# Kernel optimization log

Measured on AMD Instinct MI355X. Metric: run time of the kernel, lower is better.

## Reference

```python
import jax, jax.numpy as jnp
import numpy as np

ROPE_BASE = 10000.0
NEG_INF = -1e30


def _rope(x, pos):
    # x: [B, Hx, D], pos: [B] int32. Rotate-half RoPE (non-interleaved).
    D = x.shape[-1]
    inv_freq = 1.0 / (ROPE_BASE ** (jnp.arange(0, D, 2, dtype=jnp.float32) / D))  # [D/2]
    ang = pos.astype(jnp.float32)[:, None] * inv_freq[None, :]                    # [B, D/2]
    emb = jnp.concatenate([ang, ang], axis=-1)                                    # [B, D]
    cos = jnp.cos(emb)[:, None, :]
    sin = jnp.sin(emb)[:, None, :]
    x1, x2 = x[..., : D // 2], x[..., D // 2 :]
    rotated = jnp.concatenate([-x2, x1], axis=-1)
    return x * cos + rotated * sin


def setup_inputs() -> dict:
    key = jax.random.key(0)
    ks = jax.random.split(key, 7)
    B, H, KVH, D = 32, 32, 8, 128
    BLOCK_SIZE, MAX_BLOCKS = 16, 128
    NUM_BLOCKS = B * MAX_BLOCKS  # 4096, disjoint blocks per sequence
    MAX_CTX = BLOCK_SIZE * MAX_BLOCKS  # 2048
    query = jax.random.normal(ks[0], (B, H, D), dtype=jnp.float32)
    new_k = jax.random.normal(ks[1], (B, KVH, D), dtype=jnp.float32)
    new_v = jax.random.normal(ks[2], (B, KVH, D), dtype=jnp.float32)
    k_cache = jax.random.normal(ks[3], (NUM_BLOCKS, BLOCK_SIZE, KVH, D), dtype=jnp.float32)
    v_cache = jax.random.normal(ks[4], (NUM_BLOCKS, BLOCK_SIZE, KVH, D), dtype=jnp.float32)
    block_table = jnp.arange(B * MAX_BLOCKS, dtype=jnp.int32).reshape(B, MAX_BLOCKS)
    context_lens = jnp.clip(jax.random.randint(ks[5], (B,), 0, MAX_CTX, dtype=jnp.int32), 1, MAX_CTX)
    return {"query": query, "key": new_k, "value": new_v,
            "k_cache": k_cache, "v_cache": v_cache,
            "block_table": block_table, "context_lens": context_lens}


def reference(query, key, value, k_cache, v_cache, block_table, context_lens):
    B, H, D = query.shape
    KVH = key.shape[1]
    G = H // KVH  # GQA group size
    block_size = k_cache.shape[1]
    max_blocks = block_table.shape[1]
    S = max_blocks * block_size
    scale = D ** -0.5

    # RoPE at position = context_lens (as in the original module)
    q_rot = _rope(query, context_lens)  # [B, H, D]
    k_rot = _rope(key, context_lens)    # [B, KVH, D]

    # Store new KV at token index context_lens - 1 via block table (paged scatter)
    tok = context_lens - 1
    blk = jnp.take_along_axis(block_table, (tok // block_size)[:, None], axis=1)[:, 0]  # [B]
    off = tok % block_size
    k_cache = k_cache.at[blk, off].set(k_rot)
    v_cache = v_cache.at[blk, off].set(value)

    # Gather per-sequence pages: [B, max_blocks, block_size, KVH, D] -> [B, S, KVH, D]
    K = k_cache[block_table].reshape(B, S, KVH, D)
    V = v_cache[block_table].reshape(B, S, KVH, D)

    # Single-query attention over valid context (positions < context_lens)
    qg = q_rot.reshape(B, KVH, G, D)
    scores = jnp.einsum("bkgd,bskd->bkgs", qg, K) * scale  # [B, KVH, G, S]
    valid = jnp.arange(S, dtype=jnp.int32)[None, :] < context_lens[:, None]  # [B, S]
    scores = jnp.where(valid[:, None, None, :], scores, NEG_INF)
    probs = jax.nn.softmax(scores, axis=-1)
    out = jnp.einsum("bkgs,bskd->bkgd", probs, V).reshape(B, H, D)
    return out
```

## Files before the change

kernel.cpp:

```cpp
#include <hip/hip_runtime.h>
#include <math.h>

#define BATCH 32
#define NH 32
#define NKVH 8
#define GRP 4
#define HD 128
#define BLKSZ 16
#define MAXB 128
#define PART 128
#define NPART 16
#define SCALE 0.08838834764831845f
#define NEGINF (-1e30f)

#define WS_QROT 0
#define WS_ML   (BATCH*NH*HD)
#define WS_OP   (WS_ML + BATCH*NKVH*GRP*NPART*2)

__global__ __launch_bounds__(128)
void prep(const float* __restrict__ q,
          const float* __restrict__ nk,
          const float* __restrict__ nv,
          float* __restrict__ kc,
          float* __restrict__ vc,
          const int* __restrict__ btab,
          const int* __restrict__ ctx,
          float* __restrict__ ws) {
    int b = blockIdx.x;
    int t = threadIdx.x;
    int L = ctx[b];
    __shared__ float cs[64], sn[64];
    if (t < 64) {
        double f = pow(10000.0, -(double)t / 64.0);
        double a = (double)L * f;
        cs[t] = (float)cos(a);
        sn[t] = (float)sin(a);
    }
    __syncthreads();
    float c = cs[t & 63], s = sn[t & 63];
    for (int h = 0; h < NH; ++h) {
        const float* qp = q + ((size_t)b * NH + h) * HD;
        float x = qp[t], y = qp[t ^ 64];
        float r = (t < 64) ? (x * c - y * s) : (x * c + y * s);
        ws[WS_QROT + ((size_t)b * NH + h) * HD + t] = r * SCALE;
    }
    int tok = L - 1;
    int blk = btab[b * MAXB + (tok >> 4)];
    int off = tok & 15;
    for (int kh = 0; kh < NKVH; ++kh) {
        const float* kp = nk + ((size_t)b * NKVH + kh) * HD;
        float x = kp[t], y = kp[t ^ 64];
        float r = (t < 64) ? (x * c - y * s) : (x * c + y * s);
        size_t row = (((size_t)blk * BLKSZ + off) * NKVH + kh) * HD;
        kc[row + t] = r;
        vc[row + t] = nv[((size_t)b * NKVH + kh) * HD + t];
    }
}

__global__ __launch_bounds__(256)
void attn(const float* __restrict__ kc,
          const float* __restrict__ vc,
          const int* __restrict__ ctx,
          const int* __restrict__ btab,
          float* __restrict__ ws)
{
    int part = blockIdx.x, kvh = blockIdx.y, b = blockIdx.z;
    int L = ctx[b];
    int start = part * PART;
    if (start >= L) return;
    int end = min(start + PART, L);
    int n = end - start;

    int tid = threadIdx.x;
    int hw = tid >> 5;
    int hl = tid & 31;
    int wave = tid >> 6, lane = tid & 63;

    __shared__ int   bts[PART / BLKSZ];
    __shared__ float qs[GRP][HD];
    __shared__ float sc[GRP][PART];
    __shared__ float oacc[4][GRP][HD];

    if (tid < PART / BLKSZ)
        bts[tid] = btab[b * MAXB + (start >> 4) + tid];
    {
        const float* qrot = ws + WS_QROT + ((size_t)b * NH + kvh * GRP) * HD;
        ((float2*)&qs[0][0])[tid] = ((const float2*)qrot)[tid];
    }
    __syncthreads();

    float4 qa[GRP];
#pragma unroll
    for (int g = 0; g < GRP; ++g)
        qa[g] = *(const float4*)(&qs[g][4 * hl]);

    const size_t koff = (size_t)kvh * HD + 4 * hl;

    int i = start + hw;
    for (; i + 24 < end; i += 32) {
        int s0 = i, s1 = i + 8, s2 = i + 16, s3 = i + 24;
        float4 k0 = *(const float4*)(kc + ((size_t)bts[(s0 - start) >> 4] << 14) + ((s0 & 15) << 10) + koff);
        float4 k1 = *(const float4*)(kc + ((size_t)bts[(s1 - start) >> 4] << 14) + ((s1 & 15) << 10) + koff);
        float4 k2 = *(const float4*)(kc + ((size_t)bts[(s2 - start) >> 4] << 14) + ((s2 & 15) << 10) + koff);
        float4 k3 = *(const float4*)(kc + ((size_t)bts[(s3 - start) >> 4] << 14) + ((s3 & 15) << 10) + koff);
        float p0[GRP], p1[GRP], p2[GRP], p3[GRP];
#pragma unroll
        for (int g = 0; g < GRP; ++g) {
            p0[g] = qa[g].x * k0.x + qa[g].y * k0.y + qa[g].z * k0.z + qa[g].w * k0.w;
            p1[g] = qa[g].x * k1.x + qa[g].y * k1.y + qa[g].z * k1.z + qa[g].w * k1.w;
            p2[g] = qa[g].x * k2.x + qa[g].y * k2.y + qa[g].z * k2.z + qa[g].w * k2.w;
            p3[g] = qa[g].x * k3.x + qa[g].y * k3.y + qa[g].z * k3.z + qa[g].w * k3.w;
        }
#pragma unroll
        for (int off = 16; off >= 1; off >>= 1) {
#pragma unroll
            for (int g = 0; g < GRP; ++g) {
                p0[g] += __shfl_xor(p0[g], off, 32);
                p1[g] += __shfl_xor(p1[g], off, 32);
                p2[g] += __shfl_xor(p2[g], off, 32);
                p3[g] += __shfl_xor(p3[g], off, 32);
            }
        }
        if (hl == 0) {
#pragma unroll
            for (int g = 0; g < GRP; ++g) {
                sc[g][s0 - start] = p0[g];
                sc[g][s1 - start] = p1[g];
                sc[g][s2 - start] = p2[g];
                sc[g][s3 - start] = p3[g];
            }
        }
    }
    for (; i < end; i += 8) {
        float4 k0 = *(const float4*)(kc + ((size_t)bts[(i - start) >> 4] << 14) + ((i & 15) << 10) + koff);
        float p0[GRP];
#pragma unroll
        for (int g = 0; g < GRP; ++g)
            p0[g] = qa[g].x * k0.x + qa[g].y * k0.y + qa[g].z * k0.z + qa[g].w * k0.w;
#pragma unroll
        for (int off = 16; off >= 1; off >>= 1)
#pragma unroll
            for (int g = 0; g < GRP; ++g)
                p0[g] += __shfl_xor(p0[g], off, 32);
        if (hl == 0)
#pragma unroll
            for (int g = 0; g < GRP; ++g)
                sc[g][i - start] = p0[g];
    }
    __syncthreads();

    {
        int g = wave;
        float m = NEGINF;
        for (int j = lane; j < n; j += 64) m = fmaxf(m, sc[g][j]);
#pragma unroll
        for (int off = 32; off >= 1; off >>= 1) m = fmaxf(m, __shfl_xor(m, off));
        float sum = 0.f;
        for (int j = lane; j < n; j += 64) {
            float e = __expf(sc[g][j] - m);
            sc[g][j] = e;
            sum += e;
        }
#pragma unroll
        for (int off = 32; off >= 1; off >>= 1) sum += __shfl_xor(sum, off);
        if (lane == 0) {
            size_t mlidx = ((((size_t)b * NKVH + kvh) * GRP + g) * NPART + part) * 2;
            ws[WS_ML + mlidx]     = m;
            ws[WS_ML + mlidx + 1] = sum;
        }
    }
    __syncthreads();

    float2 acc[GRP];
#pragma unroll
    for (int g = 0; g < GRP; ++g) acc[g] = make_float2(0.f, 0.f);

    const size_t voff = (size_t)kvh * HD + 2 * lane;
    int t0 = start + (wave << 6);
    int tend = min(t0 + 64, end);
    int t = t0;
    for (; t + 3 < tend; t += 4) {
        float2 v0 = *(const float2*)(vc + ((size_t)bts[(t     - start) >> 4] << 14) + (( t      & 15) << 10) + voff);
        float2 v1 = *(const float2*)(vc + ((size_t)bts[(t + 1 - start) >> 4] << 14) + (((t + 1) & 15) << 10) + voff);
        float2 v2 = *(const float2*)(vc + ((size_t)bts[(t + 2 - start) >> 4] << 14) + (((t + 2) & 15) << 10) + voff);
        float2 v3 = *(const float2*)(vc + ((size_t)bts[(t + 3 - start) >> 4] << 14) + (((t + 3) & 15) << 10) + voff);
#pragma unroll
        for (int g = 0; g < GRP; ++g) {
            float4 e = *(const float4*)(&sc[g][t - start]);
            acc[g].x += e.x * v0.x; acc[g].y += e.x * v0.y;
            acc[g].x += e.y * v1.x; acc[g].y += e.y * v1.y;
            acc[g].x += e.z * v2.x; acc[g].y += e.z * v2.y;
            acc[g].x += e.w * v3.x; acc[g].y += e.w * v3.y;
        }
    }
    for (; t < tend; ++t) {
        float2 v0 = *(const float2*)(vc + ((size_t)bts[(t - start) >> 4] << 14) + ((t & 15) << 10) + voff);
#pragma unroll
        for (int g = 0; g < GRP; ++g) {
            float e = sc[g][t - start];
            acc[g].x += e * v0.x; acc[g].y += e * v0.y;
        }
    }
#pragma unroll
    for (int g = 0; g < GRP; ++g)
        *(float2*)&oacc[wave][g][2 * lane] = acc[g];
    __syncthreads();

    for (int o = tid; o < GRP * HD; o += 256) {
        int g = o >> 7, d = o & 127;
        float ssum = oacc[0][g][d] + oacc[1][g][d] + oacc[2][g][d] + oacc[3][g][d];
        ws[WS_OP + ((((size_t)b * NKVH + kvh) * GRP + g) * NPART + part) * HD + d] = ssum;
    }
}

__global__ __launch_bounds__(128)
void attn_reduce(const int* __restrict__ ctx,
                 const float* __restrict__ ws,
                 float* __restrict__ out) {
    int bh = blockIdx.x;
    int b = bh >> 5;
    int h = bh & 31;
    int kvh = h >> 2, g = h & 3;
    int L = ctx[b];
    int np = min(NPART, (L + PART - 1) / PART);
    size_t base = (((size_t)b * NKVH + kvh) * GRP + g) * NPART;
    float M = NEGINF;
    for (int p = 0; p < np; ++p)
        M = fmaxf(M, ws[WS_ML + (base + p) * 2]);
    float w_[NPART];
    float Lsum = 0.f;
    for (int p = 0; p < np; ++p) {
        float e = __expf(ws[WS_ML + (base + p) * 2] - M);
        w_[p] = e;
        Lsum += e * ws[WS_ML + (base + p) * 2 + 1];
    }
    float inv = 1.0f / Lsum;
    int d = threadIdx.x;
    float acc = 0.f;
    for (int p = 0; p < np; ++p)
        acc += w_[p] * ws[WS_OP + (base + p) * HD + d];
    out[((size_t)b * NH + h) * HD + d] = acc * inv;
}

extern "C" void kernel_launch(void* const* d_in, const int* in_sizes, int n_in,
                              void* d_out, int out_size, void* d_ws, size_t ws_size,
                              hipStream_t stream) {
    const float* q    = (const float*)d_in[0];
    const float* nk   = (const float*)d_in[1];
    const float* nv   = (const float*)d_in[2];
    float*       kc   = (float*)d_in[3];
    float*       vc   = (float*)d_in[4];
    const int*   btab = (const int*)d_in[5];
    const int*   ctx  = (const int*)d_in[6];
    float* out = (float*)d_out;
    float* ws  = (float*)d_ws;

    prep<<<dim3(BATCH), dim3(128), 0, stream>>>(q, nk, nv, kc, vc, btab, ctx, ws);
    attn<<<dim3(NPART, NKVH, BATCH), dim3(256), 0, stream>>>(kc, vc, ctx, btab, ws);
    attn_reduce<<<dim3(BATCH * NH), dim3(128), 0, stream>>>(ctx, ws, out);
}
```

Baseline: 490.5 us.

## Stop writing new KV into cache; inject new token in attention and use nontemporal loads

The prep kernel no longer scatters the rotated key and new value into the paged caches. It stores the rotated key in workspace, and the attention kernel handles the last token specially by reading the new key and value directly. Cache loads switch to nontemporal builtins to reduce cache pollution. This drops the in-place cache mutation, so repeated calls no longer depend on modified inputs, and it adds a small branch in the last partition.

```diff
diff --git a/kernel.cpp b/kernel.cpp
--- a/kernel.cpp
+++ b/kernel.cpp
@@ -14,16 +14,23 @@
 #define NEGINF (-1e30f)
 
 #define WS_QROT 0
-#define WS_ML   (BATCH*NH*HD)
+#define WS_KROT (BATCH*NH*HD)
+#define WS_ML   (WS_KROT + BATCH*NKVH*HD)
 #define WS_OP   (WS_ML + BATCH*NKVH*GRP*NPART*2)
+
+typedef float f32x4 __attribute__((ext_vector_type(4)));
+typedef float f32x2 __attribute__((ext_vector_type(2)));
+
+__device__ __forceinline__ f32x4 ldnt4(const float* p) {
+    return __builtin_nontemporal_load((const f32x4*)p);
+}
+__device__ __forceinline__ f32x2 ldnt2(const float* p) {
+    return __builtin_nontemporal_load((const f32x2*)p);
+}
 
 __global__ __launch_bounds__(128)
 void prep(const float* __restrict__ q,
           const float* __restrict__ nk,
-          const float* __restrict__ nv,
-          float* __restrict__ kc,
-          float* __restrict__ vc,
-          const int* __restrict__ btab,
           const int* __restrict__ ctx,
           float* __restrict__ ws) {
     int b = blockIdx.x;
@@ -44,22 +51,18 @@
         float r = (t < 64) ? (x * c - y * s) : (x * c + y * s);
         ws[WS_QROT + ((size_t)b * NH + h) * HD + t] = r * SCALE;
     }
-    int tok = L - 1;
-    int blk = btab[b * MAXB + (tok >> 4)];
-    int off = tok & 15;
     for (int kh = 0; kh < NKVH; ++kh) {
         const float* kp = nk + ((size_t)b * NKVH + kh) * HD;
         float x = kp[t], y = kp[t ^ 64];
         float r = (t < 64) ? (x * c - y * s) : (x * c + y * s);
-        size_t row = (((size_t)blk * BLKSZ + off) * NKVH + kh) * HD;
-        kc[row + t] = r;
-        vc[row + t] = nv[((size_t)b * NKVH + kh) * HD + t];
+        ws[WS_KROT + ((size_t)b * NKVH + kh) * HD + t] = r;
     }
 }
 
 __global__ __launch_bounds__(256)
 void attn(const float* __restrict__ kc,
           const float* __restrict__ vc,
+          const float* __restrict__ nv,
           const int* __restrict__ ctx,
           const int* __restrict__ btab,
           float* __restrict__ ws)
@@ -70,6 +73,8 @@
     if (start >= L) return;
     int end = min(start + PART, L);
     int n = end - start;
+    bool hasNew = (end == L);
+    int endC = end - (hasNew ? 1 : 0);
 
     int tid = threadIdx.x;
     int hw = tid >> 5;
@@ -97,12 +102,12 @@
     const size_t koff = (size_t)kvh * HD + 4 * hl;
 
     int i = start + hw;
-    for (; i + 24 < end; i += 32) {
+    for (; i + 24 < endC; i += 32) {
         int s0 = i, s1 = i + 8, s2 = i + 16, s3 = i + 24;
-        float4 k0 = *(const float4*)(kc + ((size_t)bts[(s0 - start) >> 4] << 14) + ((s0 & 15) << 10) + koff);
-        float4 k1 = *(const float4*)(kc + ((size_t)bts[(s1 - start) >> 4] << 14) + ((s1 & 15) << 10) + koff);
-        float4 k2 = *(const float4*)(kc + ((size_t)bts[(s2 - start) >> 4] << 14) + ((s2 & 15) << 10) + koff);
-        float4 k3 = *(const float4*)(kc + ((size_t)bts[(s3 - start) >> 4] << 14) + ((s3 & 15) << 10) + koff);
+        f32x4 k0 = ldnt4(kc + ((size_t)bts[(s0 - start) >> 4] << 14) + ((s0 & 15) << 10) + koff);
+        f32x4 k1 = ldnt4(kc + ((size_t)bts[(s1 - start) >> 4] << 14) + ((s1 & 15) << 10) + koff);
+        f32x4 k2 = ldnt4(kc + ((size_t)bts[(s2 - start) >> 4] << 14) + ((s2 & 15) << 10) + koff);
+        f32x4 k3 = ldnt4(kc + ((size_t)bts[(s3 - start) >> 4] << 14) + ((s3 & 15) << 10) + koff);
         float p0[GRP], p1[GRP], p2[GRP], p3[GRP];
 #pragma unroll
         for (int g = 0; g < GRP; ++g) {
@@ -131,8 +136,8 @@
             }
         }
     }
-    for (; i < end; i += 8) {
-        float4 k0 = *(const float4*)(kc + ((size_t)bts[(i - start) >> 4] << 14) + ((i & 15) << 10) + koff);
+    for (; i < endC; i += 8) {
+        f32x4 k0 = ldnt4(kc + ((size_t)bts[(i - start) >> 4] << 14) + ((i & 15) << 10) + koff);
         float p0[GRP];
 #pragma unroll
         for (int g = 0; g < GRP; ++g)
@@ -146,6 +151,17 @@
 #pragma unroll
             for (int g = 0; g < GRP; ++g)
                 sc[g][i - start] = p0[g];
+    }
+
+    if (hasNew) {
+        int g = wave;
+        const float* kn = ws + WS_KROT + ((size_t)b * NKVH + kvh) * HD;
+        float2 kv = *(const float2*)(kn + 2 * lane);
+        float2 qv = *(const float2*)(&qs[g][2 * lane]);
+        float p = qv.x * kv.x + qv.y * kv.y;
+#pragma unroll
+        for (int off = 32; off >= 1; off >>= 1) p += __shfl_xor(p, off);
+        if (lane == 0) sc[g][n - 1] = p;
     }
     __syncthreads();
 
@@ -177,13 +193,13 @@
 
     const size_t voff = (size_t)kvh * HD + 2 * lane;
     int t0 = start + (wave << 6);
-    int tend = min(t0 + 64, end);
+    int tend = min(t0 + 64, endC);
     int t = t0;
     for (; t + 3 < tend; t += 4) {
-        float2 v0 = *(const float2*)(vc + ((size_t)bts[(t     - start) >> 4] << 14) + (( t      & 15) << 10) + voff);
-        float2 v1 = *(const float2*)(vc + ((size_t)bts[(t + 1 - start) >> 4] << 14) + (((t + 1) & 15) << 10) + voff);
-        float2 v2 = *(const float2*)(vc + ((size_t)bts[(t + 2 - start) >> 4] << 14) + (((t + 2) & 15) << 10) + voff);
-        float2 v3 = *(const float2*)(vc + ((size_t)bts[(t + 3 - start) >> 4] << 14) + (((t + 3) & 15) << 10) + voff);
+        f32x2 v0 = ldnt2(vc + ((size_t)bts[(t     - start) >> 4] << 14) + (( t      & 15) << 10) + voff);
+        f32x2 v1 = ldnt2(vc + ((size_t)bts[(t + 1 - start) >> 4] << 14) + (((t + 1) & 15) << 10) + voff);
+        f32x2 v2 = ldnt2(vc + ((size_t)bts[(t + 2 - start) >> 4] << 14) + (((t + 2) & 15) << 10) + voff);
+        f32x2 v3 = ldnt2(vc + ((size_t)bts[(t + 3 - start) >> 4] << 14) + (((t + 3) & 15) << 10) + voff);
 #pragma unroll
         for (int g = 0; g < GRP; ++g) {
             float4 e = *(const float4*)(&sc[g][t - start]);
@@ -194,11 +210,19 @@
         }
     }
     for (; t < tend; ++t) {
-        float2 v0 = *(const float2*)(vc + ((size_t)bts[(t - start) >> 4] << 14) + ((t & 15) << 10) + voff);
+        f32x2 v0 = ldnt2(vc + ((size_t)bts[(t - start) >> 4] << 14) + ((t & 15) << 10) + voff);
 #pragma unroll
         for (int g = 0; g < GRP; ++g) {
             float e = sc[g][t - start];
             acc[g].x += e * v0.x; acc[g].y += e * v0.y;
+        }
+    }
+    if (hasNew && wave == ((n - 1) >> 6)) {
+        float2 v = *(const float2*)(nv + ((size_t)b * NKVH + kvh) * HD + 2 * lane);
+#pragma unroll
+        for (int g = 0; g < GRP; ++g) {
+            float e = sc[g][n - 1];
+            acc[g].x += e * v.x; acc[g].y += e * v.y;
         }
     }
 #pragma unroll
@@ -248,14 +272,14 @@
     const float* q    = (const float*)d_in[0];
     const float* nk   = (const float*)d_in[1];
     const float* nv   = (const float*)d_in[2];
-    float*       kc   = (float*)d_in[3];
-    float*       vc   = (float*)d_in[4];
+    const float* kc   = (const float*)d_in[3];
+    const float* vc   = (const float*)d_in[4];
     const int*   btab = (const int*)d_in[5];
     const int*   ctx  = (const int*)d_in[6];
     float* out = (float*)d_out;
     float* ws  = (float*)d_ws;
 
-    prep<<<dim3(BATCH), dim3(128), 0, stream>>>(q, nk, nv, kc, vc, btab, ctx, ws);
-    attn<<<dim3(NPART, NKVH, BATCH), dim3(256), 0, stream>>>(kc, vc, ctx, btab, ws);
+    prep<<<dim3(BATCH), dim3(128), 0, stream>>>(q, nk, ctx, ws);
+    attn<<<dim3(NPART, NKVH, BATCH), dim3(256), 0, stream>>>(kc, vc, nv, ctx, btab, ws);
     attn_reduce<<<dim3(BATCH * NH), dim3(128), 0, stream>>>(ctx, ws, out);
 }
```

Result: no change. 495.7 us (+1.1%).
